# Optimization experiments

Hardware: AMD Instinct MI355X
Metric: run time of the kernel (lower is better)

## Reference

```python
import jax, jax.numpy as jnp
import numpy as np

INPUT_DIM = 1024
OUTPUT_DIM = 1024
DEGREE = 8


def pentanacci_basis(x, degree):
    # x: [B, I] (already sigmoided). Returns [B, I, degree+1].
    # P0 = 0, P1 = 1, P2 = x, P3 = x, P4 = x^2,
    # Pn = x*P(n-1) + P(n-2) + P(n-3) + P(n-4) + P(n-5) for n >= 5
    zeros = jnp.zeros_like(x)
    ones = jnp.ones_like(x)
    seeds = [zeros, ones, x, x, x * x]
    basis = seeds[: degree + 1]
    for n in range(5, degree + 1):
        basis.append(x * basis[n - 1] + basis[n - 2] + basis[n - 3]
                     + basis[n - 4] + basis[n - 5])
    return jnp.stack(basis, axis=-1)


def setup_inputs() -> dict:
    key = jax.random.key(0)
    kx, kw = jax.random.split(key)
    x = jax.random.normal(kx, (4096, INPUT_DIM), dtype=jnp.float32)
    std = 1.0 / (INPUT_DIM * (DEGREE + 1))
    coeffs = std * jax.random.normal(kw, (INPUT_DIM, OUTPUT_DIM, DEGREE + 1),
                                     dtype=jnp.float32)
    return {"x": x, "coeffs": coeffs}


def reference(x, coeffs):
    degree = coeffs.shape[-1] - 1
    xs = jax.nn.sigmoid(x)                      # [B, I]
    basis = pentanacci_basis(xs, degree)        # [B, I, D+1]
    y = jnp.einsum('bid,iod->bo', basis, coeffs)  # [B, O]
    return y
```

## Files before the change

kernel.cpp:

```cpp
#include <hip/hip_runtime.h>
#include <stdint.h>

#define M_DIM 4096
#define I_DIM 1024
#define O_DIM 1024
#define KB 6
#define K_DIM (I_DIM * KB)
#define SPLITS 4

typedef __attribute__((ext_vector_type(8))) short short8;
typedef __attribute__((ext_vector_type(4))) float f32x4;
typedef __attribute__((ext_vector_type(4))) unsigned int u32x4;
typedef __attribute__((ext_vector_type(4))) float hfloat4;
typedef __attribute__((ext_vector_type(8))) _Float16 h16x8;

__device__ __forceinline__ unsigned short f2bf(float f) {
  union { float f; unsigned int u; } v; v.f = f;
  unsigned int u = v.u;
  unsigned int r = (u + 0x7FFFu + ((u >> 16) & 1u)) >> 16;
  return (unsigned short)r;
}

__global__ __launch_bounds__(256) void k_prep(const float* __restrict__ x,
                                              const float* __restrict__ C,
                                              unsigned short* __restrict__ A,
                                              unsigned short* __restrict__ Bt,
                                              float* __restrict__ partB) {
  const int bid = blockIdx.x;
  if (bid < 2048) {
    int t = bid * 256 + threadIdx.x;
    long e0 = (long)t * 8;
    const hfloat4* xp = (const hfloat4*)(x + e0);
    hfloat4 v0 = xp[0], v1 = xp[1];
    float xv[8];
    xv[0]=v0[0]; xv[1]=v0[1]; xv[2]=v0[2]; xv[3]=v0[3];
    xv[4]=v1[0]; xv[5]=v1[1]; xv[6]=v1[2]; xv[7]=v1[3];
    unsigned short outv[48];
#pragma unroll
    for (int e = 0; e < 8; ++e) {
      float s  = 1.0f / (1.0f + __expf(-xv[e]));
      float b2 = s, b3 = s, b4 = s * s;
      float b5 = fmaf(s, b4, b3 + b2 + 1.0f);
      float b6 = fmaf(s, b5, b4 + b3 + b2 + 1.0f);
      float b7 = fmaf(s, b6, b5 + b4 + b3 + b2);
      float b8 = fmaf(s, b7, b6 + b5 + b4 + b3);
      outv[e*6+0] = f2bf(s);
      outv[e*6+1] = f2bf(b4);
      outv[e*6+2] = f2bf(b5);
      outv[e*6+3] = f2bf(b6);
      outv[e*6+4] = f2bf(b7);
      outv[e*6+5] = f2bf(b8);
    }
    u32x4* dst = (u32x4*)(A + e0 * KB);
    const u32x4* srcv = (const u32x4*)outv;
#pragma unroll
    for (int q = 0; q < 6; ++q) dst[q] = srcv[q];
  } else {
    __shared__ unsigned short tile[32 * 192];
    __shared__ float bred[256];
    int b = bid - 2048;
    int i0 = (b & 31) * 32, o0 = (b >> 5) * 32;
    int t = threadIdx.x;
    int ol = t & 31, ig = t >> 5;
    float bsum = 0.f;
#pragma unroll
    for (int r = 0; r < 4; ++r) {
      int il = ig + r * 8;
      const float* p = C + (size_t)(i0 + il) * (O_DIM * 9) + (size_t)(o0 + ol) * 9;
      float c1 = p[1];
      float c2 = p[2], c3 = p[3], c4 = p[4], c5 = p[5], c6 = p[6], c7 = p[7], c8 = p[8];
      bsum += c1;
      unsigned short* q = &tile[ol * 192 + il * 6];
      q[0] = f2bf(c2 + c3);
      q[1] = f2bf(c4);
      q[2] = f2bf(c5);
      q[3] = f2bf(c6);
      q[4] = f2bf(c7);
      q[5] = f2bf(c8);
    }
    bred[t] = bsum;
    __syncthreads();
    if (t < 32) {
      float s = 0.f;
#pragma unroll
      for (int g = 0; g < 8; ++g) s += bred[g * 32 + t];
      partB[(size_t)(b & 31) * O_DIM + o0 + t] = s;
    }
    const u32x4* lsrc = (const u32x4*)tile;
#pragma unroll
    for (int r = 0; r < 3; ++r) {
      int c = t + r * 256;
      int row = c / 24, off = c % 24;
      u32x4* gdst = (u32x4*)(Bt + (size_t)(o0 + row) * K_DIM + (size_t)i0 * 6 + off * 8);
      *gdst = lsrc[c];
    }
  }
}

__global__ __launch_bounds__(256) void k_bias2(const float* __restrict__ partB,
                                               float* __restrict__ bias) {
  int o = blockIdx.x * 256 + threadIdx.x;
  float s = 0.f;
#pragma unroll
  for (int ib = 0; ib < 32; ++ib) s += partB[(size_t)ib * O_DIM + o];
  bias[o] = s;
}

#define SBAR __builtin_amdgcn_sched_barrier(0)

template<bool SPLIT>
__global__ __launch_bounds__(512, 2) void k_gemm8(const unsigned short* __restrict__ A,
                                                  const unsigned short* __restrict__ B,
                                                  const float* __restrict__ bias,
                                                  void* __restrict__ dst) {
  constexpr int CK = SPLIT ? (K_DIM / SPLITS) : K_DIM;
  constexpr int NT = CK / 64;
  constexpr int PPX = SPLIT ? 8 : 2;
  __shared__ char lds[131072];
  const int tid = threadIdx.x;
  const int lane = tid & 63, wid = tid >> 6;
  const int wm = wid >> 2, wn = wid & 3;
  const int l15 = lane & 15, lk = lane >> 4, l7 = lane & 7;
  const int flat = blockIdx.x + (blockIdx.y << 2) + (blockIdx.z << 6);
  const int xcd = flat & 7, slot = flat >> 3;
  const int panel = xcd * PPX + (slot >> 2);
  const int xn = slot & 3;
  const int ym = panel & 15, zk = panel >> 4;
  const int m0 = ym * 256, n0 = xn * 256;
  const size_t kb = (size_t)zk * CK;
  const int srow = tid >> 3;
  const int cg8 = (((tid & 7) ^ ((tid >> 3) & 7)) * 8);
  const int cx0 = (lk ^ l7) * 16;
  const int cx1 = ((4 + lk) ^ l7) * 16;
  const int arow = wm * 128 + l15;
  const int brow = wn * 64 + l15;

  auto gload = [&](const unsigned short* s, int ldsoff) {
    __builtin_amdgcn_global_load_lds((const __attribute__((address_space(1))) void*)s,
        (__attribute__((address_space(3))) void*)(lds + ldsoff), 16, 0, 0);
  };
  auto stageA = [&](int buf, int h, int kt2) {
    const unsigned short* s = A + (size_t)(m0 + h * 128 + srow) * K_DIM + kb + (size_t)kt2 * 64 + cg8;
    int d = buf * 65536 + h * 16384 + tid * 16;
    gload(s, d);
    gload(s + (size_t)64 * K_DIM, d + 8192);
  };
  auto stageB = [&](int buf, int h, int kt2) {
    const unsigned short* s = B + (size_t)(n0 + h * 128 + srow) * K_DIM + kb + (size_t)kt2 * 64 + cg8;
    int d = buf * 65536 + 32768 + h * 16384 + tid * 16;
    gload(s, d);
    gload(s + (size_t)64 * K_DIM, d + 8192);
  };

  short8 af[4][2], bf0[2][2], bf1[2][2];
  f32x4 acc[8][4];
#pragma unroll
  for (int i = 0; i < 8; ++i)
#pragma unroll
    for (int n = 0; n < 4; ++n)
#pragma unroll
      for (int j = 0; j < 4; ++j) acc[i][n][j] = 0.f;

  auto loadA = [&](int buf, int h) {
#pragma unroll
    for (int mm = 0; mm < 4; ++mm) {
      int rb = buf * 65536 + (arow + h * 64 + mm * 16) * 128;
      af[mm][0] = *(const short8*)(lds + rb + cx0);
      af[mm][1] = *(const short8*)(lds + rb + cx1);
    }
  };
  auto loadB = [&](int buf, int g, short8 (&bfx)[2][2]) {
#pragma unroll
    for (int nn = 0; nn < 2; ++nn) {
      int rb = buf * 65536 + 32768 + (brow + g * 32 + nn * 16) * 128;
      bfx[nn][0] = *(const short8*)(lds + rb + cx0);
      bfx[nn][1] = *(const short8*)(lds + rb + cx1);
    }
  };
  auto quad = [&](int h, int g, short8 (&bfx)[2][2]) {
#pragma unroll
    for (int mm = 0; mm < 4; ++mm)
#pragma unroll
      for (int nn = 0; nn < 2; ++nn)
#pragma unroll
        for (int kc = 0; kc < 2; ++kc)
          acc[h * 4 + mm][g * 2 + nn] =
              __builtin_amdgcn_mfma_f32_16x16x32_bf16(af[mm][kc], bfx[nn][kc],
                                                      acc[h * 4 + mm][g * 2 + nn], 0, 0, 0);
  };
  auto sync1 = [&]() {
    SBAR; __builtin_amdgcn_s_barrier();
    asm volatile("s_waitcnt lgkmcnt(0)" ::: "memory"); SBAR;
    __builtin_amdgcn_s_setprio(1);
  };
  auto endp = [&]() {
    __builtin_amdgcn_s_setprio(0); SBAR;
  };

  stageA(0, 0, 0); stageA(0, 1, 0); stageB(0, 0, 0); stageB(0, 1, 0);
  stageB(1, 0, 1); stageB(1, 1, 1);
  asm volatile("s_waitcnt vmcnt(4)" ::: "memory"); SBAR;
  __builtin_amdgcn_s_barrier(); SBAR;

#pragma unroll 1
  for (int kt = 0; kt < NT; ++kt) {
    const int buf = kt & 1, nb = buf ^ 1;
    loadA(buf, 0); loadB(buf, 0, bf0);
    if (kt + 1 < NT) stageA(nb, 1, kt + 1);
    sync1(); quad(0, 0, bf0); endp();
    loadB(buf, 1, bf1);
    if (kt + 1 < NT) stageA(nb, 0, kt + 1);
    sync1(); quad(0, 1, bf1); endp();
    loadA(buf, 1);
    if (kt + 2 < NT) stageB(buf, 0, kt + 2);
    sync1(); quad(1, 1, bf1); endp();
    if (kt + 2 < NT) stageB(buf, 1, kt + 2);
    sync1(); quad(1, 0, bf0); endp();
    if (kt + 1 < NT) {
      if (kt + 2 < NT) asm volatile("s_waitcnt vmcnt(4)" ::: "memory");
      else             asm volatile("s_waitcnt vmcnt(0)" ::: "memory");
      SBAR;
      __builtin_amdgcn_s_barrier(); SBAR;
    }
  }

  if (SPLIT) {
    _Float16* base = (_Float16*)dst + (size_t)zk * ((size_t)M_DIM * O_DIM);
#pragma unroll
    for (int mi = 0; mi < 8; ++mi) {
      int r0 = m0 + wm * 128 + mi * 16 + (lk << 2);
#pragma unroll
      for (int ni = 0; ni < 4; ++ni) {
        int col = n0 + wn * 64 + ni * 16 + l15;
#pragma unroll
        for (int j = 0; j < 4; ++j)
          base[(size_t)(r0 + j) * O_DIM + col] = (_Float16)acc[mi][ni][j];
      }
    }
  } else {
    float* base = (float*)dst;
#pragma unroll
    for (int mi = 0; mi < 8; ++mi) {
      int r0 = m0 + wm * 128 + mi * 16 + (lk << 2);
#pragma unroll
      for (int ni = 0; ni < 4; ++ni) {
        int col = n0 + wn * 64 + ni * 16 + l15;
        float bv = bias[col];
#pragma unroll
        for (int j = 0; j < 4; ++j)
          base[(size_t)(r0 + j) * O_DIM + col] = acc[mi][ni][j] + bv;
      }
    }
  }
}

__global__ __launch_bounds__(256) void k_reduce(const _Float16* __restrict__ part,
                                                const float* __restrict__ bias,
                                                float* __restrict__ out) {
  size_t t = (size_t)blockIdx.x * 256 + threadIdx.x;
  size_t idx = t * 8;
  const size_t P = (size_t)M_DIM * O_DIM;
  h16x8 s0 = *(const h16x8*)(part + idx);
  h16x8 s1 = *(const h16x8*)(part + P + idx);
  h16x8 s2 = *(const h16x8*)(part + 2 * P + idx);
  h16x8 s3 = *(const h16x8*)(part + 3 * P + idx);
  size_t bo = idx & (O_DIM - 1);
  f32x4 b0 = *(const f32x4*)(bias + bo);
  f32x4 b1 = *(const f32x4*)(bias + bo + 4);
  f32x4 r0, r1;
#pragma unroll
  for (int j = 0; j < 4; ++j) {
    r0[j] = (((float)s0[j] + (float)s1[j]) + ((float)s2[j] + (float)s3[j])) + b0[j];
    r1[j] = (((float)s0[j+4] + (float)s1[j+4]) + ((float)s2[j+4] + (float)s3[j+4])) + b1[j];
  }
  *(f32x4*)(out + idx) = r0;
  *(f32x4*)(out + idx + 4) = r1;
}

extern "C" void kernel_launch(void* const* d_in, const int* in_sizes, int n_in,
                              void* d_out, int out_size, void* d_ws, size_t ws_size,
                              hipStream_t stream) {
  const float* x      = (const float*)d_in[0];
  const float* coeffs = (const float*)d_in[1];
  float* out = (float*)d_out;
  char* ws = (char*)d_ws;
  const size_t offA     = 0;
  const size_t offB     = 50331648;
  const size_t offBias  = offB + 12582912;
  const size_t offPartB = offBias + 4096;
  const size_t offPart  = offPartB + 131072;
  const size_t needSplit = offPart + (size_t)SPLITS * M_DIM * O_DIM * 2;

  unsigned short* A  = (unsigned short*)(ws + offA);
  unsigned short* Bt = (unsigned short*)(ws + offB);
  float* bias        = (float*)(ws + offBias);
  float* partB       = (float*)(ws + offPartB);
  _Float16* part     = (_Float16*)(ws + offPart);

  k_prep<<<3072, 256, 0, stream>>>(x, coeffs, A, Bt, partB);
  k_bias2<<<4, 256, 0, stream>>>(partB, bias);

  if (ws_size >= needSplit) {
    k_gemm8<true><<<dim3(O_DIM / 256, M_DIM / 256, SPLITS), 512, 0, stream>>>(A, Bt, bias, (void*)part);
    k_reduce<<<(M_DIM * O_DIM) / (256 * 8), 256, 0, stream>>>(part, bias, out);
  } else {
    k_gemm8<false><<<dim3(O_DIM / 256, M_DIM / 256, 1), 512, 0, stream>>>(A, Bt, bias, (void*)out);
  }
}
```

Before: 88.77 us.

## Replace staggered four-phase pipeline with simple double-buffered stage-then-compute loop

Drops the fine-grained schedule that interleaved partial A/B global-to-LDS stages with four barrier-separated MFMA quads and a two-tile-ahead B prefetch. Each iteration now issues all next-tile loads up front, reads all A/B fragments from LDS into two A register sets, runs all MFMAs, then waits for vmcnt(0) and takes a single barrier. This cuts the barrier count per iteration and simplifies ordering, at the cost of more live registers and less overlap between memory waits and compute. With the prefetch depth reduced to one tile, global latency may be exposed more often.

```diff
diff --git a/kernel.cpp b/kernel.cpp
--- a/kernel.cpp
+++ b/kernel.cpp
@@ -152,7 +152,7 @@
     gload(s + (size_t)64 * K_DIM, d + 8192);
   };
 
-  short8 af[4][2], bf0[2][2], bf1[2][2];
+  short8 af0[4][2], af1[4][2], bf0[2][2], bf1[2][2];
   f32x4 acc[8][4];
 #pragma unroll
   for (int i = 0; i < 8; ++i)
@@ -161,12 +161,12 @@
 #pragma unroll
       for (int j = 0; j < 4; ++j) acc[i][n][j] = 0.f;
 
-  auto loadA = [&](int buf, int h) {
+  auto loadA = [&](int buf, int h, short8 (&afx)[4][2]) {
 #pragma unroll
     for (int mm = 0; mm < 4; ++mm) {
       int rb = buf * 65536 + (arow + h * 64 + mm * 16) * 128;
-      af[mm][0] = *(const short8*)(lds + rb + cx0);
-      af[mm][1] = *(const short8*)(lds + rb + cx1);
+      afx[mm][0] = *(const short8*)(lds + rb + cx0);
+      afx[mm][1] = *(const short8*)(lds + rb + cx1);
     }
   };
   auto loadB = [&](int buf, int g, short8 (&bfx)[2][2]) {
@@ -177,7 +177,7 @@
       bfx[nn][1] = *(const short8*)(lds + rb + cx1);
     }
   };
-  auto quad = [&](int h, int g, short8 (&bfx)[2][2]) {
+  auto quad = [&](short8 (&afx)[4][2], int h, int g, short8 (&bfx)[2][2]) {
 #pragma unroll
     for (int mm = 0; mm < 4; ++mm)
 #pragma unroll
@@ -185,41 +185,29 @@
 #pragma unroll
         for (int kc = 0; kc < 2; ++kc)
           acc[h * 4 + mm][g * 2 + nn] =
-              __builtin_amdgcn_mfma_f32_16x16x32_bf16(af[mm][kc], bfx[nn][kc],
+              __builtin_amdgcn_mfma_f32_16x16x32_bf16(afx[mm][kc], bfx[nn][kc],
                                                       acc[h * 4 + mm][g * 2 + nn], 0, 0, 0);
   };
-  auto sync1 = [&]() {
-    SBAR; __builtin_amdgcn_s_barrier();
-    asm volatile("s_waitcnt lgkmcnt(0)" ::: "memory"); SBAR;
-    __builtin_amdgcn_s_setprio(1);
-  };
-  auto endp = [&]() {
-    __builtin_amdgcn_s_setprio(0); SBAR;
-  };
 
   stageA(0, 0, 0); stageA(0, 1, 0); stageB(0, 0, 0); stageB(0, 1, 0);
-  stageB(1, 0, 1); stageB(1, 1, 1);
-  asm volatile("s_waitcnt vmcnt(4)" ::: "memory"); SBAR;
+  asm volatile("s_waitcnt vmcnt(0)" ::: "memory"); SBAR;
   __builtin_amdgcn_s_barrier(); SBAR;
 
 #pragma unroll 1
   for (int kt = 0; kt < NT; ++kt) {
     const int buf = kt & 1, nb = buf ^ 1;
-    loadA(buf, 0); loadB(buf, 0, bf0);
-    if (kt + 1 < NT) stageA(nb, 1, kt + 1);
-    sync1(); quad(0, 0, bf0); endp();
-    loadB(buf, 1, bf1);
-    if (kt + 1 < NT) stageA(nb, 0, kt + 1);
-    sync1(); quad(0, 1, bf1); endp();
-    loadA(buf, 1);
-    if (kt + 2 < NT) stageB(buf, 0, kt + 2);
-    sync1(); quad(1, 1, bf1); endp();
-    if (kt + 2 < NT) stageB(buf, 1, kt + 2);
-    sync1(); quad(1, 0, bf0); endp();
     if (kt + 1 < NT) {
-      if (kt + 2 < NT) asm volatile("s_waitcnt vmcnt(4)" ::: "memory");
-      else             asm volatile("s_waitcnt vmcnt(0)" ::: "memory");
-      SBAR;
+      stageA(nb, 0, kt + 1); stageA(nb, 1, kt + 1);
+      stageB(nb, 0, kt + 1); stageB(nb, 1, kt + 1);
+    }
+    loadA(buf, 0, af0); loadB(buf, 0, bf0);
+    loadB(buf, 1, bf1); loadA(buf, 1, af1);
+    __builtin_amdgcn_s_setprio(1);
+    quad(af0, 0, 0, bf0); quad(af0, 0, 1, bf1);
+    quad(af1, 1, 1, bf1); quad(af1, 1, 0, bf0);
+    __builtin_amdgcn_s_setprio(0); SBAR;
+    if (kt + 1 < NT) {
+      asm volatile("s_waitcnt vmcnt(0)" ::: "memory"); SBAR;
       __builtin_amdgcn_s_barrier(); SBAR;
     }
   }
```

Result: no change. 88.23 us (-0.6%).
